# Optimization experiments

Measured on AMD Instinct MI355X. Metric: run time of the kernel, lower is better.

The kernel has to match this reference:

```python
import jax, jax.numpy as jnp
import numpy as np

CHUNK = 256  # rows of z processed per scan step; keeps [CHUNK, M, D] intermediate ~64MB


def setup_inputs() -> dict:
    key = jax.random.key(0)
    k1, k2, k3, k4 = jax.random.split(key, 4)
    N, M, D = 2048, 512, 128
    z = jax.random.normal(k1, (N, D), dtype=jnp.float32)
    e = jax.random.normal(k2, (M, D), dtype=jnp.float32)
    probs = jax.random.uniform(k3, (N,), dtype=jnp.float32)
    dropout = jax.random.uniform(k4, (N, D), dtype=jnp.float32)
    return {"z": z, "e": e, "probs": probs, "dropout": dropout}


def reference(z, e, probs, dropout):
    # z: [N, D], e: [M, D]
    N, D = z.shape
    M = e.shape[0]
    nchunk = N // CHUNK

    def body(carry, zc):
        # zc: [CHUNK, D]
        min_sum, min_elem = carry  # [M], [M, D]
        # elementwise squared differences for this chunk: [CHUNK, M, D]
        delem = (zc[:, None, :] - e[None, :, :]) ** 2
        dsum = jnp.sum(delem, axis=2)                      # [CHUNK, M]
        min_sum = jnp.minimum(min_sum, jnp.min(dsum, axis=0))
        min_elem = jnp.minimum(min_elem, jnp.min(delem, axis=0))
        return (min_sum, min_elem), None

    init = (jnp.full((M,), jnp.inf, dtype=z.dtype),
            jnp.full((M, D), jnp.inf, dtype=z.dtype))
    (min_sum, min_elem), _ = jax.lax.scan(body, init, z.reshape(nchunk, CHUNK, D))

    # torch: mean over M of min over N of sum_d distance
    min_loss = jnp.mean(min_sum)
    # torch: mean over (M, D) of elementwise min over N
    wise_min_loss = jnp.mean(min_elem)

    # z = z * (dropout < probs[:, None])  -- boolean mask multiply
    z_out = z * (dropout < probs[:, None]).astype(z.dtype)
    return min_loss, wise_min_loss, z_out
```

## Files before the change

kernel.cpp:

```cpp
#include <hip/hip_runtime.h>


#define N_ 2048
#define M_ 512
#define D_ 128
#define PB_SUM  (8 * M_ * D_)
#define ACC_OFF (PB_SUM + M_ * 32)
#define CNT_OFF (ACC_OFF + 2)

__global__ void __launch_bounds__(256, 4) k_main(
        const float* __restrict__ z, const float* __restrict__ e,
        const float* __restrict__ probs, const float* __restrict__ drop,
        float* __restrict__ out, float* __restrict__ ws) {
    const int bx = blockIdx.x;
    const int t  = threadIdx.x;

    if (bx < 256) {
        const int mg = bx >> 3, chunk = bx & 7;
        const int d = t & 127, half = t >> 7;
        const int m0 = mg * 16 + half * 8;
        const int n0 = chunk * 256;

        float ev[8], mn[8];
        #pragma unroll
        for (int k = 0; k < 8; ++k) {
            ev[k] = e[(m0 + k) * D_ + d];
            mn[k] = __uint_as_float(0x7f800000u);
        }
        const float* zp = z + n0 * D_ + d;
        #pragma unroll 8
        for (int i = 0; i < 256; ++i) {
            float zv = zp[i * D_];
            #pragma unroll
            for (int k = 0; k < 8; ++k) {
                float df = zv - ev[k];
                mn[k] = fminf(mn[k], df * df);
            }
        }
        float* pe = ws + (size_t)chunk * (M_ * D_) + m0 * D_ + d;
        #pragma unroll
        for (int k = 0; k < 8; ++k) pe[k * D_] = mn[k];
    } else if (bx < 512) {
        const int b = bx - 256;
        const int nb = b >> 5, mt = b & 31;
        const int n = nb * 256 + t;
        const int m0 = mt * 16;

        float s[16];
        #pragma unroll
        for (int k = 0; k < 16; ++k) s[k] = 0.f;

        const float4* z4 = reinterpret_cast<const float4*>(z) + n * 32;
        const float4* e4 = reinterpret_cast<const float4*>(e);

        #pragma unroll 1
        for (int dc = 0; dc < 4; ++dc) {
            float4 zq[8];
            #pragma unroll
            for (int jj = 0; jj < 8; ++jj) zq[jj] = z4[dc * 8 + jj];
            #pragma unroll
            for (int k = 0; k < 16; ++k) {
                const float4* ep = e4 + (m0 + k) * 32 + dc * 8;
                float a0 = 0.f, a1 = 0.f, a2 = 0.f, a3 = 0.f;
                #pragma unroll
                for (int jj = 0; jj < 8; ++jj) {
                    float4 evq = ep[jj];
                    float dx = zq[jj].x - evq.x; a0 = fmaf(dx, dx, a0);
                    float dy = zq[jj].y - evq.y; a1 = fmaf(dy, dy, a1);
                    float dz = zq[jj].z - evq.z; a2 = fmaf(dz, dz, a2);
                    float dw = zq[jj].w - evq.w; a3 = fmaf(dw, dw, a3);
                }
                s[k] += (a0 + a1) + (a2 + a3);
            }
        }
        #pragma unroll
        for (int off = 32; off; off >>= 1) {
            #pragma unroll
            for (int k = 0; k < 16; ++k)
                s[k] = fminf(s[k], __shfl_xor(s[k], off));
        }
        if ((t & 63) == 0) {
            const int w = t >> 6;
            #pragma unroll
            for (int k = 0; k < 16; ++k)
                ws[PB_SUM + (m0 + k) * 32 + nb * 4 + w] = s[k];
        }
    } else {
        const int b = bx - 512;
        const int i = b * 256 + t;
        const int n = i >> 5;
        const float p = probs[n];
        const float4 zv = reinterpret_cast<const float4*>(z)[i];
        const float4 dv = reinterpret_cast<const float4*>(drop)[i];
        float2 lo, hi;
        lo.x = dv.x < p ? zv.x : 0.f;
        lo.y = dv.y < p ? zv.y : 0.f;
        hi.x = dv.z < p ? zv.z : 0.f;
        hi.y = dv.w < p ? zv.w : 0.f;
        float2* o = reinterpret_cast<float2*>(out + 2) + i * 2;
        o[0] = lo;
        o[1] = hi;
        if (b == 0 && t == 0) {
            ws[ACC_OFF] = 0.f;
            ws[ACC_OFF + 1] = 0.f;
            reinterpret_cast<unsigned int*>(ws)[CNT_OFF] = 0u;
        }
    }
}

__device__ __forceinline__ float min4(float4 v) {
    return fminf(fminf(v.x, v.y), fminf(v.z, v.w));
}

__global__ void __launch_bounds__(256) k_fin(float* __restrict__ ws,
                                             float* __restrict__ out) {
    const int b = blockIdx.x, t = threadIdx.x;
    float* acc = ws + ACC_OFF;
    unsigned int* cnt = reinterpret_cast<unsigned int*>(ws) + CNT_OFF;

    const int cell = b * 1024 + t * 4;
    float4 mv = *reinterpret_cast<const float4*>(ws + cell);
    #pragma unroll
    for (int c = 1; c < 8; ++c) {
        float4 v = *reinterpret_cast<const float4*>(ws + c * (M_ * D_) + cell);
        mv.x = fminf(mv.x, v.x); mv.y = fminf(mv.y, v.y);
        mv.z = fminf(mv.z, v.z); mv.w = fminf(mv.w, v.w);
    }
    float s_elem = (mv.x + mv.y) + (mv.z + mv.w);

    float s_sum = 0.f;
    if (t < 64) {
        const int m = b * 8 + (t >> 3);
        const int j = t & 7;
        float4 v = *reinterpret_cast<const float4*>(ws + PB_SUM + m * 32 + j * 4);
        float mn = min4(v);
        mn = fminf(mn, __shfl_xor(mn, 1));
        mn = fminf(mn, __shfl_xor(mn, 2));
        mn = fminf(mn, __shfl_xor(mn, 4));
        if ((t & 7) == 0) s_sum = mn;
    }

    #pragma unroll
    for (int off = 32; off; off >>= 1) {
        s_elem += __shfl_xor(s_elem, off);
        s_sum  += __shfl_xor(s_sum, off);
    }
    __shared__ float sm[8];
    const int w = t >> 6;
    if ((t & 63) == 0) { sm[w] = s_elem; sm[4 + w] = s_sum; }
    __syncthreads();
    if (t == 0) {
        float te = sm[0] + sm[1] + sm[2] + sm[3];
        float ts = sm[4] + sm[5] + sm[6] + sm[7];
        atomicAdd(&acc[0], ts);
        atomicAdd(&acc[1], te);
        __threadfence();
        unsigned int old = atomicAdd(cnt, 1u);
        if (old == 63u) {
            float a0 = atomicAdd(&acc[0], 0.f);
            float a1 = atomicAdd(&acc[1], 0.f);
            out[0] = a0 * (1.0f / 512.0f);
            out[1] = a1 * (1.0f / 65536.0f);
        }
    }
}

extern "C" void kernel_launch(void* const* d_in, const int* in_sizes, int n_in,
                              void* d_out, int out_size, void* d_ws, size_t ws_size,
                              hipStream_t stream) {
    const float* z     = (const float*)d_in[0];
    const float* e     = (const float*)d_in[1];
    const float* probs = (const float*)d_in[2];
    const float* drop  = (const float*)d_in[3];
    float* out = (float*)d_out;
    float* ws  = (float*)d_ws;

    k_main<<<dim3(768), dim3(256), 0, stream>>>(z, e, probs, drop, out, ws);
    k_fin<<<dim3(64), dim3(256), 0, stream>>>(ws, out);
}
```

Measured before the change: 91.24 us.

## Use packed FP32 math in distance kernels and move masking into finalize kernel

Rewrites both distance loops with inline v_pk_add/mul/fma_f32 packed two-wide FP32 instructions, so each instruction handles two rows or two dimensions and VALU instruction count drops. The dropout-mask pass moves from the main kernel into the finalize kernel, and the accumulator reset moves to block 0 of the main kernel. Launch bounds go from 4 to 2 waves, allowing more registers per thread. Risks are lower occupancy and inline asm that blocks compiler scheduling.

After: 92.92 us. About the same (+1.8%).

```diff
diff --git a/kernel.cpp b/kernel.cpp
--- a/kernel.cpp
+++ b/kernel.cpp
@@ -8,10 +8,11 @@
 #define ACC_OFF (PB_SUM + M_ * 32)
 #define CNT_OFF (ACC_OFF + 2)
 
-__global__ void __launch_bounds__(256, 4) k_main(
+typedef float v2f __attribute__((ext_vector_type(2)));
+
+__global__ void __launch_bounds__(256, 2) k_part(
         const float* __restrict__ z, const float* __restrict__ e,
-        const float* __restrict__ probs, const float* __restrict__ drop,
-        float* __restrict__ out, float* __restrict__ ws) {
+        float* __restrict__ ws) {
     const int bx = blockIdx.x;
     const int t  = threadIdx.x;
 
@@ -21,58 +22,75 @@
         const int m0 = mg * 16 + half * 8;
         const int n0 = chunk * 256;
 
-        float ev[8], mn[8];
+        v2f nege[8];
+        float mnx[8], mny[8];
         #pragma unroll
         for (int k = 0; k < 8; ++k) {
-            ev[k] = e[(m0 + k) * D_ + d];
-            mn[k] = __uint_as_float(0x7f800000u);
+            float evk = e[(m0 + k) * D_ + d];
+            nege[k].x = -evk; nege[k].y = -evk;
+            mnx[k] = __uint_as_float(0x7f800000u);
+            mny[k] = mnx[k];
         }
         const float* zp = z + n0 * D_ + d;
         #pragma unroll 8
-        for (int i = 0; i < 256; ++i) {
-            float zv = zp[i * D_];
+        for (int i = 0; i < 128; ++i) {
+            v2f zz;
+            zz.x = zp[(2 * i) * D_];
+            zz.y = zp[(2 * i + 1) * D_];
             #pragma unroll
             for (int k = 0; k < 8; ++k) {
-                float df = zv - ev[k];
-                mn[k] = fminf(mn[k], df * df);
+                v2f dd, sq;
+                asm("v_pk_add_f32 %0, %1, %2" : "=v"(dd) : "v"(zz), "v"(nege[k]));
+                asm("v_pk_mul_f32 %0, %1, %1" : "=v"(sq) : "v"(dd));
+                mnx[k] = fminf(mnx[k], sq.x);
+                mny[k] = fminf(mny[k], sq.y);
             }
         }
         float* pe = ws + (size_t)chunk * (M_ * D_) + m0 * D_ + d;
         #pragma unroll
-        for (int k = 0; k < 8; ++k) pe[k * D_] = mn[k];
-    } else if (bx < 512) {
+        for (int k = 0; k < 8; ++k) pe[k * D_] = fminf(mnx[k], mny[k]);
+
+        if (bx == 0 && t == 0) {
+            ws[ACC_OFF] = 0.f;
+            ws[ACC_OFF + 1] = 0.f;
+            reinterpret_cast<unsigned int*>(ws)[CNT_OFF] = 0u;
+        }
+    } else {
         const int b = bx - 256;
         const int nb = b >> 5, mt = b & 31;
         const int n = nb * 256 + t;
         const int m0 = mt * 16;
 
-        float s[16];
-        #pragma unroll
-        for (int k = 0; k < 16; ++k) s[k] = 0.f;
-
-        const float4* z4 = reinterpret_cast<const float4*>(z) + n * 32;
-        const float4* e4 = reinterpret_cast<const float4*>(e);
+        v2f s2[16];
+        #pragma unroll
+        for (int k = 0; k < 16; ++k) { s2[k].x = 0.f; s2[k].y = 0.f; }
+        v2f mone; mone.x = -1.f; mone.y = -1.f;
+
+        const v2f* z2p = reinterpret_cast<const v2f*>(z) + n * 64;
+        const v2f* e2p = reinterpret_cast<const v2f*>(e);
 
         #pragma unroll 1
-        for (int dc = 0; dc < 4; ++dc) {
-            float4 zq[8];
-            #pragma unroll
-            for (int jj = 0; jj < 8; ++jj) zq[jj] = z4[dc * 8 + jj];
+        for (int dc = 0; dc < 8; ++dc) {
+            v2f zz[8];
+            #pragma unroll
+            for (int jj = 0; jj < 8; ++jj) zz[jj] = z2p[dc * 8 + jj];
             #pragma unroll
             for (int k = 0; k < 16; ++k) {
-                const float4* ep = e4 + (m0 + k) * 32 + dc * 8;
-                float a0 = 0.f, a1 = 0.f, a2 = 0.f, a3 = 0.f;
+                const v2f* ep = e2p + (m0 + k) * 64 + dc * 8;
                 #pragma unroll
                 for (int jj = 0; jj < 8; ++jj) {
-                    float4 evq = ep[jj];
-                    float dx = zq[jj].x - evq.x; a0 = fmaf(dx, dx, a0);
-                    float dy = zq[jj].y - evq.y; a1 = fmaf(dy, dy, a1);
-                    float dz = zq[jj].z - evq.z; a2 = fmaf(dz, dz, a2);
-                    float dw = zq[jj].w - evq.w; a3 = fmaf(dw, dw, a3);
+                    v2f ev = ep[jj];
+                    v2f dd;
+                    asm("v_pk_fma_f32 %0, %1, %2, %3"
+                        : "=v"(dd) : "v"(ev), "v"(mone), "v"(zz[jj]));
+                    asm("v_pk_fma_f32 %0, %1, %1, %0"
+                        : "+v"(s2[k]) : "v"(dd));
                 }
-                s[k] += (a0 + a1) + (a2 + a3);
             }
         }
+        float s[16];
+        #pragma unroll
+        for (int k = 0; k < 16; ++k) s[k] = s2[k].x + s2[k].y;
         #pragma unroll
         for (int off = 32; off; off >>= 1) {
             #pragma unroll
@@ -85,8 +103,21 @@
             for (int k = 0; k < 16; ++k)
                 ws[PB_SUM + (m0 + k) * 32 + nb * 4 + w] = s[k];
         }
-    } else {
-        const int b = bx - 512;
+    }
+}
+
+__device__ __forceinline__ float min4(float4 v) {
+    return fminf(fminf(v.x, v.y), fminf(v.z, v.w));
+}
+
+__global__ void __launch_bounds__(256, 2) k_post(
+        const float* __restrict__ z, const float* __restrict__ probs,
+        const float* __restrict__ drop, float* __restrict__ ws,
+        float* __restrict__ out) {
+    const int bx = blockIdx.x, t = threadIdx.x;
+
+    if (bx >= 64) {
+        const int b = bx - 64;
         const int i = b * 256 + t;
         const int n = i >> 5;
         const float p = probs[n];
@@ -100,21 +131,10 @@
         float2* o = reinterpret_cast<float2*>(out + 2) + i * 2;
         o[0] = lo;
         o[1] = hi;
-        if (b == 0 && t == 0) {
-            ws[ACC_OFF] = 0.f;
-            ws[ACC_OFF + 1] = 0.f;
-            reinterpret_cast<unsigned int*>(ws)[CNT_OFF] = 0u;
-        }
-    }
-}
-
-__device__ __forceinline__ float min4(float4 v) {
-    return fminf(fminf(v.x, v.y), fminf(v.z, v.w));
-}
-
-__global__ void __launch_bounds__(256) k_fin(float* __restrict__ ws,
-                                             float* __restrict__ out) {
-    const int b = blockIdx.x, t = threadIdx.x;
+        return;
+    }
+
+    const int b = bx;
     float* acc = ws + ACC_OFF;
     unsigned int* cnt = reinterpret_cast<unsigned int*>(ws) + CNT_OFF;
 
@@ -175,6 +195,6 @@
     float* out = (float*)d_out;
     float* ws  = (float*)d_ws;
 
-    k_main<<<dim3(768), dim3(256), 0, stream>>>(z, e, probs, drop, out, ws);
-    k_fin<<<dim3(64), dim3(256), 0, stream>>>(ws, out);
-}
+    k_part<<<dim3(512), dim3(256), 0, stream>>>(z, e, ws);
+    k_post<<<dim3(320), dim3(256), 0, stream>>>(z, probs, drop, ws, out);
+}
```

## Use packed float2 math in min-elem and distance-sum branches

Applied to the files above, without the earlier changes.

Rewrites the elementwise-min and the distance-sum branches to use two-wide float vectors, so the compiler can emit packed FP32 subtract, multiply, FMA and min instructions. The elementwise branch now has each thread cover two D columns and 32 M rows per block, which halves its block count to 128 and shrinks the grid from 768 to 640 blocks. Launch bounds drop from 4 to 3 blocks per SM to leave room for more registers. The aim is to double ALU throughput on the compute-bound branches, at the cost of fewer blocks and lower occupancy.

Result: slower. 93.19 us (+2.1%).

```diff
diff --git a/kernel.cpp b/kernel.cpp
--- a/kernel.cpp
+++ b/kernel.cpp
@@ -8,47 +8,54 @@
 #define ACC_OFF (PB_SUM + M_ * 32)
 #define CNT_OFF (ACC_OFF + 2)
 
-__global__ void __launch_bounds__(256, 4) k_main(
+typedef float v2f __attribute__((ext_vector_type(2)));
+
+__global__ void __launch_bounds__(256, 3) k_part(
         const float* __restrict__ z, const float* __restrict__ e,
         const float* __restrict__ probs, const float* __restrict__ drop,
         float* __restrict__ out, float* __restrict__ ws) {
     const int bx = blockIdx.x;
     const int t  = threadIdx.x;
 
-    if (bx < 256) {
+    if (bx < 128) {
         const int mg = bx >> 3, chunk = bx & 7;
-        const int d = t & 127, half = t >> 7;
-        const int m0 = mg * 16 + half * 8;
+        const int dp = t & 63;
+        const int sub = t >> 6;
+        const int m0 = mg * 32 + sub * 8;
         const int n0 = chunk * 256;
 
-        float ev[8], mn[8];
+        v2f ev[8], mn[8];
+        const v2f inf2 = { __uint_as_float(0x7f800000u),
+                           __uint_as_float(0x7f800000u) };
         #pragma unroll
         for (int k = 0; k < 8; ++k) {
-            ev[k] = e[(m0 + k) * D_ + d];
-            mn[k] = __uint_as_float(0x7f800000u);
+            ev[k] = *reinterpret_cast<const v2f*>(e + (m0 + k) * D_ + 2 * dp);
+            mn[k] = inf2;
         }
-        const float* zp = z + n0 * D_ + d;
-        #pragma unroll 8
+        const v2f* zp = reinterpret_cast<const v2f*>(z + n0 * D_) + dp;
+        #pragma unroll 4
         for (int i = 0; i < 256; ++i) {
-            float zv = zp[i * D_];
+            v2f zz = zp[i * 64];
             #pragma unroll
             for (int k = 0; k < 8; ++k) {
-                float df = zv - ev[k];
-                mn[k] = fminf(mn[k], df * df);
+                v2f dd = zz - ev[k];
+                v2f sq = dd * dd;
+                mn[k] = __builtin_elementwise_min(mn[k], sq);
             }
         }
-        float* pe = ws + (size_t)chunk * (M_ * D_) + m0 * D_ + d;
+        float* pe = ws + (size_t)chunk * (M_ * D_) + m0 * D_ + 2 * dp;
         #pragma unroll
-        for (int k = 0; k < 8; ++k) pe[k * D_] = mn[k];
-    } else if (bx < 512) {
-        const int b = bx - 256;
+        for (int k = 0; k < 8; ++k)
+            *reinterpret_cast<v2f*>(pe + k * D_) = mn[k];
+    } else if (bx < 384) {
+        const int b = bx - 128;
         const int nb = b >> 5, mt = b & 31;
         const int n = nb * 256 + t;
         const int m0 = mt * 16;
 
-        float s[16];
+        v2f acc[16];
         #pragma unroll
-        for (int k = 0; k < 16; ++k) s[k] = 0.f;
+        for (int k = 0; k < 16; ++k) acc[k] = (v2f)0.f;
 
         const float4* z4 = reinterpret_cast<const float4*>(z) + n * 32;
         const float4* e4 = reinterpret_cast<const float4*>(e);
@@ -61,18 +68,25 @@
             #pragma unroll
             for (int k = 0; k < 16; ++k) {
                 const float4* ep = e4 + (m0 + k) * 32 + dc * 8;
-                float a0 = 0.f, a1 = 0.f, a2 = 0.f, a3 = 0.f;
+                v2f ca = (v2f)0.f, cb = (v2f)0.f;
                 #pragma unroll
                 for (int jj = 0; jj < 8; ++jj) {
                     float4 evq = ep[jj];
-                    float dx = zq[jj].x - evq.x; a0 = fmaf(dx, dx, a0);
-                    float dy = zq[jj].y - evq.y; a1 = fmaf(dy, dy, a1);
-                    float dz = zq[jj].z - evq.z; a2 = fmaf(dz, dz, a2);
-                    float dw = zq[jj].w - evq.w; a3 = fmaf(dw, dw, a3);
+                    v2f zlo = { zq[jj].x, zq[jj].y };
+                    v2f zhi = { zq[jj].z, zq[jj].w };
+                    v2f elo = { evq.x, evq.y };
+                    v2f ehi = { evq.z, evq.w };
+                    v2f d0 = zlo - elo;
+                    ca += d0 * d0;
+                    v2f d1 = zhi - ehi;
+                    cb += d1 * d1;
                 }
-                s[k] += (a0 + a1) + (a2 + a3);
+                acc[k] += ca + cb;
             }
         }
+        float s[16];
+        #pragma unroll
+        for (int k = 0; k < 16; ++k) s[k] = acc[k].x + acc[k].y;
         #pragma unroll
         for (int off = 32; off; off >>= 1) {
             #pragma unroll
@@ -86,7 +100,7 @@
                 ws[PB_SUM + (m0 + k) * 32 + nb * 4 + w] = s[k];
         }
     } else {
-        const int b = bx - 512;
+        const int b = bx - 384;
         const int i = b * 256 + t;
         const int n = i >> 5;
         const float p = probs[n];
@@ -175,6 +189,6 @@
     float* out = (float*)d_out;
     float* ws  = (float*)d_ws;
 
-    k_main<<<dim3(768), dim3(256), 0, stream>>>(z, e, probs, drop, out, ws);
+    k_part<<<dim3(640), dim3(256), 0, stream>>>(z, e, probs, drop, out, ws);
     k_fin<<<dim3(64), dim3(256), 0, stream>>>(ws, out);
 }
```
